# Optimization experiments

Measured on AMD Instinct MI355X. Metric: run time of the kernel, lower is better.

The kernel has to match this reference:

```python
import jax, jax.numpy as jnp
import numpy as np

B, S, C = 2, 2048, 1024
U, H = 1024, 16
FFH = int(U * 4.0)
NEG = -1e9
EPS = 1e-5


def setup_inputs() -> dict:
    key = jax.random.key(0)
    ks = jax.random.split(key, 16)
    w = lambda k, sh: jax.random.normal(k, sh, dtype=jnp.float32) * 0.02
    return {
        'x': jax.random.normal(ks[0], (B, S, C), dtype=jnp.float32),
        'wq': w(ks[1], (C, U)), 'bq': jnp.zeros((U,), jnp.float32),
        'wk': w(ks[2], (C, U)), 'bk': jnp.zeros((U,), jnp.float32),
        'wv': w(ks[3], (C, U)), 'bv': jnp.zeros((U,), jnp.float32),
        'wf1': w(ks[4], (U, FFH)), 'bf1': jnp.zeros((FFH,), jnp.float32),
        'wf2': w(ks[5], (FFH, U)), 'bf2': jnp.zeros((U,), jnp.float32),
        'ln_g': jnp.ones((S, U), jnp.float32), 'ln_b': jnp.zeros((S, U), jnp.float32),
        'ffln_g': jnp.ones((S, U), jnp.float32), 'ffln_b': jnp.zeros((S, U), jnp.float32),
    }


def _ln2d(x, g, b):
    # LayerNorm over last two dims ([len_ts, units]) as in nn.LayerNorm([S, U])
    m = jnp.mean(x, axis=(-2, -1), keepdims=True)
    v = jnp.mean(jnp.square(x - m), axis=(-2, -1), keepdims=True)
    return (x - m) * jax.lax.rsqrt(v + EPS) * g + b


def reference(x, wq, bq, wk, bk, wv, bv, wf1, bf1, wf2, bf2, ln_g, ln_b, ffln_g, ffln_b):
    dh = U // H
    Q = (x @ wq + bq).reshape(B, S, H, dh)
    K = (x @ wk + bk).reshape(B, S, H, dh)
    V = (x @ wv + bv).reshape(B, S, H, dh)
    scores = jnp.einsum('bqhd,bkhd->bhqk', Q, K) / jnp.sqrt(jnp.float32(dh))
    mask = jnp.tril(jnp.ones((S, S), dtype=bool))  # causal tril buffer
    scores = jnp.where(mask, scores, NEG)
    attn = jax.nn.softmax(scores, axis=-1)
    out = jnp.einsum('bhqk,bkhd->bqhd', attn, V).reshape(B, S, U)
    out = out + x  # residual
    out = _ln2d(out, ln_g, ln_b)
    ff = jax.nn.relu(out @ wf1 + bf1) @ wf2 + bf2
    out = _ln2d(out + ff, ffln_g, ffln_b)
    return out
```

## Files before the change

kernel.cpp:

```cpp
#include <hip/hip_runtime.h>
#include <hip/hip_bf16.h>

typedef short s16x8 __attribute__((ext_vector_type(8)));
typedef float f32x4 __attribute__((ext_vector_type(4)));
typedef float f32x16 __attribute__((ext_vector_type(16)));
typedef unsigned short u16x4 __attribute__((ext_vector_type(4)));
typedef unsigned u32x4 __attribute__((ext_vector_type(4)));

#define DEV static __device__ __forceinline__

DEV unsigned short f2bf(float f) {
  __hip_bfloat16 h = __float2bfloat16(f);
  return *reinterpret_cast<unsigned short*>(&h);
}
DEV float bf2f(unsigned short u) {
  union { unsigned u; float f; } v; v.u = (unsigned)u << 16; return v.f;
}

#define GLDS16(src, dst) \
  __builtin_amdgcn_global_load_lds((const __attribute__((address_space(1))) void*)(src), \
                                   (__attribute__((address_space(3))) void*)(dst), 16, 0, 0)

#define MFMA(a, b, c) __builtin_amdgcn_mfma_f32_16x16x32_bf16((a), (b), (c), 0, 0, 0)
#define MFMA32(a, b, c) __builtin_amdgcn_mfma_f32_32x32x16_bf16((a), (b), (c), 0, 0, 0)

__global__ __launch_bounds__(256) void k_f32_to_bf16(const float* __restrict__ in,
                                                     unsigned short* __restrict__ out, int n4) {
  int i = blockIdx.x * 256 + threadIdx.x;
  if (i >= n4) return;
  float4 v = ((const float4*)in)[i];
  u16x4 o; o.x = f2bf(v.x); o.y = f2bf(v.y); o.z = f2bf(v.z); o.w = f2bf(v.w);
  ((u16x4*)out)[i] = o;
}

__global__ __launch_bounds__(256) void k_transpose_w(const float* __restrict__ W,
                                                     unsigned short* __restrict__ Wt,
                                                     int K, int N, float scale) {
  __shared__ float t[64][65];
  int k0 = blockIdx.x * 64, n0 = blockIdx.y * 64;
  int tid = threadIdx.x;
#pragma unroll
  for (int i = 0; i < 16; ++i) {
    int idx = tid + i * 256; int r = idx >> 6, c = idx & 63;
    t[r][c] = W[(size_t)(k0 + r) * N + (n0 + c)];
  }
  __syncthreads();
#pragma unroll
  for (int i = 0; i < 16; ++i) {
    int idx = tid + i * 256; int r = idx >> 6, c = idx & 63;
    Wt[(size_t)(n0 + r) * K + (k0 + c)] = f2bf(t[c][r] * scale);
  }
}

__global__ void k_concat3(const float* __restrict__ a, const float* __restrict__ b,
                          const float* __restrict__ c, float* __restrict__ out, int n, float sa) {
  int i = blockIdx.x * 256 + threadIdx.x;
  if (i >= 3 * n) return;
  int j = (i < n) ? i : (i < 2 * n ? i - n : i - 2 * n);
  out[i] = (i < n) ? a[j] * sa : (i < 2 * n ? b[j] : c[j]);
}

template <int MODE>
__global__ __launch_bounds__(512, 2) void k_gemm8(
    const unsigned short* __restrict__ A, int lda,
    const unsigned short* __restrict__ Bt, int ldb,
    const float* __restrict__ bias,
    unsigned short* __restrict__ Cb, float* __restrict__ Cf, int ldc,
    int K, int nnt, size_t zstride,
    unsigned short* __restrict__ Cq, unsigned short* __restrict__ Ck,
    unsigned short* __restrict__ Cv) {
  __shared__ __align__(16) unsigned short As[2 * 2 * 8192];
  __shared__ __align__(16) unsigned short Bs[2 * 2 * 8192];
  int nwg = gridDim.x;
  int bid = blockIdx.x;
  int cpx = nwg >> 3;
  int swz = (bid & 7) * cpx + (bid >> 3);
  int mt = swz / nnt, nt = swz % nnt;
  int m0 = mt * 256, n0 = nt * 256;
  int tid = threadIdx.x, w = tid >> 6, l = tid & 63;
  int wm = (w >> 2) * 128, wn = (w & 3) * 64;
  int kb = blockIdx.z * K;

  int sr = tid >> 2;
  int gsrc = (tid & 3) ^ ((sr >> 1) & 3);
  const unsigned short* Ag0 = A + (size_t)(m0 + sr) * lda + kb + gsrc * 8;
  const unsigned short* Ag1 = Ag0 + (size_t)128 * lda;
  const unsigned short* Bg0 = Bt + (size_t)(n0 + sr) * ldb + kb + gsrc * 8;
  const unsigned short* Bg1 = Bg0 + (size_t)128 * ldb;

#define STG_A(t, kh) do { int _c = (t) * 64 + (kh) * 32; int _d = ((((t) & 1) * 2 + (kh)) * 8192); \
    GLDS16(Ag0 + _c, &As[_d + tid * 8]); GLDS16(Ag1 + _c, &As[_d + 4096 + tid * 8]); } while (0)
#define STG_B(t, kh) do { int _c = (t) * 64 + (kh) * 32; int _d = ((((t) & 1) * 2 + (kh)) * 8192); \
    GLDS16(Bg0 + _c, &Bs[_d + tid * 8]); GLDS16(Bg1 + _c, &Bs[_d + 4096 + tid * 8]); } while (0)

  int lswz = (l >> 1) & 3;
  int acol = ((l >> 4) ^ lswz) * 8;
  const unsigned short* Afr = &As[(wm + (l & 15)) * 32 + acol];
  const unsigned short* Bfr = &Bs[(wn + (l & 15)) * 32 + acol];

  f32x4 acc[8][4] = {};
  int nkt = K >> 6;

  STG_A(0, 0); STG_B(0, 0); STG_A(0, 1); STG_B(0, 1); STG_A(1, 0); STG_B(1, 0);
  asm volatile("s_waitcnt vmcnt(4)" ::: "memory");
  __builtin_amdgcn_s_barrier();
  __builtin_amdgcn_sched_barrier(0);

  for (int t = 0; t < nkt; ++t) {
    int cur = t & 1, rem = nkt - t;
    const unsigned short* ab = Afr + cur * 16384;
    const unsigned short* bb = Bfr + cur * 16384;
    s16x8 af[4], bf[4];
    if (t + 1 < nkt) STG_A(t + 1, 1);
#pragma unroll
    for (int nr = 0; nr < 4; ++nr) bf[nr] = *(const s16x8*)(bb + nr * 512);
#pragma unroll
    for (int mr = 0; mr < 4; ++mr) af[mr] = *(const s16x8*)(ab + mr * 512);
    __builtin_amdgcn_s_setprio(1);
#pragma unroll
    for (int mr = 0; mr < 4; ++mr)
#pragma unroll
      for (int nr = 0; nr < 4; ++nr)
        acc[mr][nr] = MFMA(af[mr], bf[nr], acc[mr][nr]);
    __builtin_amdgcn_s_setprio(0);
    if (t + 1 < nkt) STG_B(t + 1, 1);
#pragma unroll
    for (int mr = 0; mr < 4; ++mr) af[mr] = *(const s16x8*)(ab + 2048 + mr * 512);
    __builtin_amdgcn_s_setprio(1);
#pragma unroll
    for (int mr = 0; mr < 4; ++mr)
#pragma unroll
      for (int nr = 0; nr < 4; ++nr)
        acc[mr + 4][nr] = MFMA(af[mr], bf[nr], acc[mr + 4][nr]);
    __builtin_amdgcn_s_setprio(0);
    if (rem >= 2) { asm volatile("s_waitcnt vmcnt(4)" ::: "memory"); }
    else          { asm volatile("s_waitcnt vmcnt(0)" ::: "memory"); }
    __builtin_amdgcn_s_barrier();
    __builtin_amdgcn_sched_barrier(0);
    if (t + 2 < nkt) STG_A(t + 2, 0);
#pragma unroll
    for (int nr = 0; nr < 4; ++nr) bf[nr] = *(const s16x8*)(bb + 8192 + nr * 512);
#pragma unroll
    for (int mr = 0; mr < 4; ++mr) af[mr] = *(const s16x8*)(ab + 8192 + mr * 512);
    __builtin_amdgcn_s_setprio(1);
#pragma unroll
    for (int mr = 0; mr < 4; ++mr)
#pragma unroll
      for (int nr = 0; nr < 4; ++nr)
        acc[mr][nr] = MFMA(af[mr], bf[nr], acc[mr][nr]);
    __builtin_amdgcn_s_setprio(0);
    if (t + 2 < nkt) STG_B(t + 2, 0);
#pragma unroll
    for (int mr = 0; mr < 4; ++mr) af[mr] = *(const s16x8*)(ab + 8192 + 2048 + mr * 512);
    __builtin_amdgcn_s_setprio(1);
#pragma unroll
    for (int mr = 0; mr < 4; ++mr)
#pragma unroll
      for (int nr = 0; nr < 4; ++nr)
        acc[mr + 4][nr] = MFMA(af[mr], bf[nr], acc[mr + 4][nr]);
    __builtin_amdgcn_s_setprio(0);
    if (rem >= 3) { asm volatile("s_waitcnt vmcnt(4)" ::: "memory"); }
    else          { asm volatile("s_waitcnt vmcnt(0)" ::: "memory"); }
    __builtin_amdgcn_s_barrier();
    __builtin_amdgcn_sched_barrier(0);
  }
#undef STG_A
#undef STG_B

  if (MODE == 4) {
    if (nt < 8) {
      unsigned short* dst = (nt < 4) ? Cq : Ck;
      int cb = (nt < 4) ? 0 : 1024;
#pragma unroll
      for (int mr = 0; mr < 8; ++mr) {
        int rb = m0 + wm + mr * 16 + (l >> 4) * 4;
#pragma unroll
        for (int nr = 0; nr < 4; ++nr) {
          int col = n0 + wn + nr * 16 + (l & 15);
          float bv = bias[col];
#pragma unroll
          for (int j = 0; j < 4; ++j)
            dst[(size_t)(rb + j) * 1024 + (col - cb)] = f2bf(acc[mr][nr][j] + bv);
        }
      }
    } else {
#pragma unroll
      for (int mr = 0; mr < 8; ++mr) {
        int rb = m0 + wm + mr * 16 + (l >> 4) * 4;
        int b2 = rb >> 11, s2 = rb & 2047;
        int s2p = (s2 & ~12) | ((s2 & 4) << 1) | ((s2 & 8) >> 1);
#pragma unroll
        for (int nr = 0; nr < 4; ++nr) {
          int col2 = n0 - 2048 + wn + nr * 16 + (l & 15);
          float bv = bias[col2 + 2048];
          u16x4 pk;
#pragma unroll
          for (int j = 0; j < 4; ++j) ((unsigned short*)&pk)[j] = f2bf(acc[mr][nr][j] + bv);
          *(u16x4*)(Cv + ((size_t)((b2 * 16 + (col2 >> 6)) * 64 + (col2 & 63))) * 2048 + s2p) = pk;
        }
      }
    }
    return;
  }
  unsigned short* Cbz = (MODE == 3) ? (Cb + zstride * blockIdx.z) : Cb;
#pragma unroll
  for (int mr = 0; mr < 8; ++mr) {
    int rb = m0 + wm + mr * 16 + (l >> 4) * 4;
#pragma unroll
    for (int nr = 0; nr < 4; ++nr) {
      int col = n0 + wn + nr * 16 + (l & 15);
      float bv = (MODE == 3) ? 0.f : bias[col];
#pragma unroll
      for (int j = 0; j < 4; ++j) {
        float v = acc[mr][nr][j] + bv;
        size_t off = (size_t)(rb + j) * ldc + col;
        if (MODE == 1) v = fmaxf(v, 0.f);
        Cbz[off] = f2bf(v);
      }
    }
  }
}

__global__ __launch_bounds__(256) void k_ff2_reduce(
    unsigned short* __restrict__ slices, const float* __restrict__ bias,
    const unsigned short* __restrict__ resid, float* __restrict__ partials) {
  __shared__ float red[8];
  int i = blockIdx.x;
  size_t rb = (size_t)i * 4096;
  int c = threadIdx.x * 4;
  u16x4 a0 = *(const u16x4*)(slices + rb + c);
  u16x4 a1 = *(const u16x4*)(slices + rb + 1024 + c);
  u16x4 a2 = *(const u16x4*)(slices + rb + 2048 + c);
  u16x4 a3 = *(const u16x4*)(slices + rb + 3072 + c);
  float4 bv = *(const float4*)(bias + c);
  u16x4 rv = *(const u16x4*)(resid + (size_t)i * 1024 + c);
  float4 o;
  o.x = bf2f(a0.x) + bf2f(a1.x) + bf2f(a2.x) + bf2f(a3.x) + bv.x + bf2f(rv.x);
  o.y = bf2f(a0.y) + bf2f(a1.y) + bf2f(a2.y) + bf2f(a3.y) + bv.y + bf2f(rv.y);
  o.z = bf2f(a0.z) + bf2f(a1.z) + bf2f(a2.z) + bf2f(a3.z) + bv.z + bf2f(rv.z);
  o.w = bf2f(a0.w) + bf2f(a1.w) + bf2f(a2.w) + bf2f(a3.w) + bv.w + bf2f(rv.w);
  __syncthreads();
  *(float4*)((float*)slices + (size_t)i * 2048 + c) = o;
  float bsum = o.x + o.y + o.z + o.w;
  float bsq = o.x * o.x + o.y * o.y + o.z * o.z + o.w * o.w;
  int wv = threadIdx.x >> 6, lv = threadIdx.x & 63;
#pragma unroll
  for (int mk = 1; mk < 64; mk <<= 1) { bsum += __shfl_xor(bsum, mk); bsq += __shfl_xor(bsq, mk); }
  if (lv == 0) { red[wv] = bsum; red[4 + wv] = bsq; }
  __syncthreads();
  if (threadIdx.x == 0) {
    partials[i * 2] = red[0] + red[1] + red[2] + red[3];
    partials[i * 2 + 1] = red[4] + red[5] + red[6] + red[7];
  }
}

__global__ __launch_bounds__(128, 2) void k_attn(
    const unsigned short* __restrict__ Qg, const unsigned short* __restrict__ Kg,
    const unsigned short* __restrict__ Vt,
    const float* __restrict__ x, unsigned short* __restrict__ hpre,
    float* __restrict__ partials, int S, int H) {
  __shared__ __align__(16) unsigned short Ks[2][4096];
  __shared__ __align__(16) unsigned short Vs[2][4096];
  __shared__ float ascr[2][32];
  __shared__ float red[4];
  int bh = blockIdx.x, b = bh >> 4, h = bh & 15;
  const int nqt = S / 64;
  int qt = nqt - 1 - (int)blockIdx.y;
  int tid = threadIdx.x, w = tid >> 6, l = tid & 63;
  int lo = l & 31, hi5 = l >> 5;
  const int U = H * 64;
  const unsigned short* Qb = Qg + (size_t)(b * S) * 1024 + h * 64;
  const unsigned short* Kb = Kg + (size_t)(b * S) * 1024 + h * 64;
  const unsigned short* Vb = Vt + (size_t)bh * 64 * S;

  int sg_r[4], sg_c[4];
#pragma unroll
  for (int it = 0; it < 4; ++it) {
    int g = it * 128 + tid;
    sg_r[it] = g >> 3;
    sg_c[it] = ((g & 7) ^ ((g >> 3) & 7)) * 8;
  }
#define STG_K(kt) do { int _kn = (kt) * 64, _bf = (kt) & 1; \
    _Pragma("unroll") for (int it = 0; it < 4; ++it) \
      GLDS16(Kb + (size_t)(_kn + sg_r[it]) * 1024 + sg_c[it], &Ks[_bf][(it * 128 + tid) * 8]); } while (0)
#define STG_V(kt) do { int _kn = (kt) * 64, _bf = (kt) & 1; \
    _Pragma("unroll") for (int it = 0; it < 4; ++it) \
      GLDS16(Vb + (size_t)sg_r[it] * S + _kn + sg_c[it], &Vs[_bf][(it * 128 + tid) * 8]); } while (0)

  int qrow = qt * 64 + w * 32 + lo;
  s16x8 qf[4];
#pragma unroll
  for (int s = 0; s < 4; ++s)
    qf[s] = *(const s16x8*)(Qb + (size_t)qrow * 1024 + s * 16 + hi5 * 8);

  int krow[16];
#pragma unroll
  for (int r = 0; r < 16; ++r) krow[r] = (r & 3) + 8 * (r >> 2) + 4 * hi5;

  f32x16 o0 = {}, o1 = {};
  float m = -1e30f, lsum = 0.f;
  f32x16 scA0, scA1, scB0, scB1;

#define QK_T(S0, S1, T) do { \
    S0 = (f32x16)(0.0f); S1 = (f32x16)(0.0f); \
    const unsigned short* _kp = &Ks[(T) & 1][0]; \
    __builtin_amdgcn_s_setprio(1); \
    _Pragma("unroll") for (int s = 0; s < 4; ++s) { \
      int gc = ((2 * s + hi5) ^ (lo & 7)) * 8; \
      s16x8 kf0 = *(const s16x8*)&_kp[lo * 64 + gc]; \
      s16x8 kf1 = *(const s16x8*)&_kp[(32 + lo) * 64 + gc]; \
      S0 = MFMA32(kf0, qf[s], S0); \
      S1 = MFMA32(kf1, qf[s], S1); } \
    __builtin_amdgcn_s_setprio(0); } while (0)

#define SMPV(S0, S1, T, DOMASK) do { \
    if (DOMASK) { int wq = w * 32 + lo; \
      _Pragma("unroll") for (int r = 0; r < 16; ++r) { \
        if (krow[r] > wq) S0[r] = -1e30f; \
        if (krow[r] + 32 > wq) S1[r] = -1e30f; } } \
    float mx = S0[0]; \
    _Pragma("unroll") for (int r = 1; r < 16; ++r) mx = fmaxf(mx, S0[r]); \
    _Pragma("unroll") for (int r = 0; r < 16; ++r) mx = fmaxf(mx, S1[r]); \
    mx = fmaxf(mx, __shfl_xor(mx, 32)); \
    if (__ballot(mx > m + 11.5415603f)) { \
      float mnew = fmaxf(m, mx); \
      float alpha = __builtin_amdgcn_exp2f(m - mnew); \
      m = mnew; lsum *= alpha; \
      if (l < 32) ascr[w][lo] = alpha; \
      _Pragma("unroll") for (int r = 0; r < 16; ++r) { \
        float aj = ascr[w][krow[r]]; o0[r] *= aj; o1[r] *= aj; } } \
    float rs = 0.f; unsigned wk0[8], wk1[8]; \
    _Pragma("unroll") for (int j = 0; j < 8; ++j) { \
      float p0 = __builtin_amdgcn_exp2f(S0[2 * j] - m); \
      float p1 = __builtin_amdgcn_exp2f(S0[2 * j + 1] - m); \
      rs += p0 + p1; wk0[j] = (unsigned)f2bf(p0) | ((unsigned)f2bf(p1) << 16); \
      float p2 = __builtin_amdgcn_exp2f(S1[2 * j] - m); \
      float p3 = __builtin_amdgcn_exp2f(S1[2 * j + 1] - m); \
      rs += p2 + p3; wk1[j] = (unsigned)f2bf(p2) | ((unsigned)f2bf(p3) << 16); } \
    rs += __shfl_xor(rs, 32); lsum += rs; \
    __builtin_amdgcn_s_setprio(1); \
    _Pragma("unroll") for (int s = 0; s < 4; ++s) { \
      u32x4 paw; \
      if (s == 0)      { paw.x = wk0[0]; paw.y = wk0[1]; paw.z = wk0[2]; paw.w = wk0[3]; } \
      else if (s == 1) { paw.x = wk0[4]; paw.y = wk0[5]; paw.z = wk0[6]; paw.w = wk0[7]; } \
      else if (s == 2) { paw.x = wk1[0]; paw.y = wk1[1]; paw.z = wk1[2]; paw.w = wk1[3]; } \
      else             { paw.x = wk1[4]; paw.y = wk1[5]; paw.z = wk1[6]; paw.w = wk1[7]; } \
      s16x8 pa = *(s16x8*)&paw; \
      int gc = ((2 * s + hi5) ^ (lo & 7)) * 8; \
      s16x8 vf0 = *(const s16x8*)&Vs[(T) & 1][lo * 64 + gc]; \
      s16x8 vf1 = *(const s16x8*)&Vs[(T) & 1][(32 + lo) * 64 + gc]; \
      o0 = MFMA32(pa, vf0, o0); \
      o1 = MFMA32(pa, vf1, o1); } \
    __builtin_amdgcn_s_setprio(0); \
  } while (0)

#define BODY(O0, O1, I0, I1, T) do { \
    asm volatile("s_waitcnt vmcnt(4)" ::: "memory"); \
    __builtin_amdgcn_s_barrier(); \
    __builtin_amdgcn_sched_barrier(0); \
    if ((T) + 1 <= qt) STG_K((T) + 1); \
    QK_T(O0, O1, (T)); \
    SMPV(I0, I1, (T) - 1, false); \
    asm volatile("s_waitcnt lgkmcnt(0)" ::: "memory"); \
    __builtin_amdgcn_sched_barrier(0); \
    __builtin_amdgcn_s_barrier(); \
    __builtin_amdgcn_sched_barrier(0); \
    if ((T) + 1 <= qt) STG_V((T) + 1); \
  } while (0)

  STG_K(0); STG_V(0);
  if (qt >= 1) {
    STG_K(1); STG_V(1);
    asm volatile("s_waitcnt vmcnt(8)" ::: "memory");
  } else {
    asm volatile("s_waitcnt vmcnt(4)" ::: "memory");
  }
  __builtin_amdgcn_s_barrier();
  __builtin_amdgcn_sched_barrier(0);
  QK_T(scA0, scA1, 0);
  asm volatile("s_waitcnt lgkmcnt(0)" ::: "memory");
  __builtin_amdgcn_sched_barrier(0);

  int t = 1;
  for (; t + 1 <= qt; t += 2) {
    BODY(scB0, scB1, scA0, scA1, t);
    BODY(scA0, scA1, scB0, scB1, t + 1);
  }
  if (t <= qt) {
    BODY(scB0, scB1, scA0, scA1, t);
    asm volatile("s_waitcnt vmcnt(0)" ::: "memory");
    __builtin_amdgcn_sched_barrier(0);
    SMPV(scB0, scB1, qt, true);
  } else {
    asm volatile("s_waitcnt vmcnt(0)" ::: "memory");
    __builtin_amdgcn_sched_barrier(0);
    SMPV(scA0, scA1, qt, true);
  }

  if (l < 32) ascr[w][lo] = 1.f / lsum;
  float bsum = 0.f, bsq = 0.f;
  unsigned short* hb = hpre + (size_t)(b * S) * U + h * 64;
  const float* xb = x + (size_t)(b * S) * U + h * 64;
#pragma unroll
  for (int r = 0; r < 16; ++r) {
    float inv = ascr[w][krow[r]];
    int srow = qt * 64 + w * 32 + krow[r];
    size_t base = (size_t)srow * U + lo;
    float v0 = o0[r] * inv + xb[base];
    float v1 = o1[r] * inv + xb[base + 32];
    hb[base] = f2bf(v0);
    hb[base + 32] = f2bf(v1);
    bsum += v0 + v1; bsq += v0 * v0 + v1 * v1;
  }
#pragma unroll
  for (int mk = 1; mk < 64; mk <<= 1) { bsum += __shfl_xor(bsum, mk); bsq += __shfl_xor(bsq, mk); }
  if (l == 0) { red[w * 2] = bsum; red[w * 2 + 1] = bsq; }
  __syncthreads();
  if (tid == 0) {
    int pi = b * (H * nqt) + h * nqt + qt;
    partials[pi * 2] = red[0] + red[2];
    partials[pi * 2 + 1] = red[1] + red[3];
  }
#undef STG_K
#undef STG_V
#undef QK_T
#undef SMPV
#undef BODY
}

__global__ __launch_bounds__(256) void k_ln_stats(const float* __restrict__ partials, int nper,
                                                  float* __restrict__ stats, float invN) {
  int b = blockIdx.x, tid = threadIdx.x;
  float s = 0.f, q = 0.f;
  for (int i = tid; i < nper; i += 256) { s += partials[(b * nper + i) * 2]; q += partials[(b * nper + i) * 2 + 1]; }
#pragma unroll
  for (int mk = 1; mk < 64; mk <<= 1) { s += __shfl_xor(s, mk); q += __shfl_xor(q, mk); }
  __shared__ float red[8];
  int w = tid >> 6, l = tid & 63;
  if (l == 0) { red[w] = s; red[4 + w] = q; }
  __syncthreads();
  if (tid == 0) {
    s = red[0] + red[1] + red[2] + red[3];
    q = red[4] + red[5] + red[6] + red[7];
    float m = s * invN, var = q * invN - m * m;
    stats[b * 2] = m; stats[b * 2 + 1] = rsqrtf(var + 1e-5f);
  }
}

__global__ __launch_bounds__(256) void k_ln_apply_b(
    const unsigned short* __restrict__ src, const float* __restrict__ stats,
    const float* __restrict__ g, const float* __restrict__ bt,
    unsigned short* __restrict__ outb, int SU) {
  int b = blockIdx.y;
  int idx = (blockIdx.x * 256 + threadIdx.x) * 4;
  float m = stats[b * 2], r = stats[b * 2 + 1];
  u16x4 v4 = *(const u16x4*)(src + (size_t)b * SU + idx);
  float4 gg = *(const float4*)(g + idx);
  float4 bb = *(const float4*)(bt + idx);
  u16x4 ob;
  ob.x = f2bf((bf2f(v4.x) - m) * r * gg.x + bb.x);
  ob.y = f2bf((bf2f(v4.y) - m) * r * gg.y + bb.y);
  ob.z = f2bf((bf2f(v4.z) - m) * r * gg.z + bb.z);
  ob.w = f2bf((bf2f(v4.w) - m) * r * gg.w + bb.w);
  *(u16x4*)(outb + (size_t)b * SU + idx) = ob;
}

__global__ __launch_bounds__(256) void k_ln_apply2(
    const float* __restrict__ src, const float* __restrict__ stats,
    const float* __restrict__ g, const float* __restrict__ bt,
    float* __restrict__ outf) {
  int b = blockIdx.y;
  int row = blockIdx.x;
  int grow = b * 2048 + row;
  int c = threadIdx.x * 4;
  float m = stats[b * 2], r = stats[b * 2 + 1];
  float4 v = *(const float4*)(src + (size_t)grow * 2048 + c);
  float4 gg = *(const float4*)(g + (size_t)row * 1024 + c);
  float4 bb = *(const float4*)(bt + (size_t)row * 1024 + c);
  float4 o;
  o.x = (v.x - m) * r * gg.x + bb.x;
  o.y = (v.y - m) * r * gg.y + bb.y;
  o.z = (v.z - m) * r * gg.z + bb.z;
  o.w = (v.w - m) * r * gg.w + bb.w;
  *(float4*)(outf + (size_t)grow * 1024 + c) = o;
}

extern "C" void kernel_launch(void* const* d_in, const int* in_sizes, int n_in,
                              void* d_out, int out_size, void* d_ws, size_t ws_size,
                              hipStream_t stream) {
  (void)in_sizes; (void)n_in; (void)out_size; (void)ws_size;
  const int S = 2048, H = 16;
  const float* x   = (const float*)d_in[0];
  const float* wq  = (const float*)d_in[1];
  const float* bq  = (const float*)d_in[2];
  const float* wk  = (const float*)d_in[3];
  const float* bk  = (const float*)d_in[4];
  const float* wv  = (const float*)d_in[5];
  const float* bv  = (const float*)d_in[6];
  const float* wf1 = (const float*)d_in[7];
  const float* bf1 = (const float*)d_in[8];
  const float* wf2 = (const float*)d_in[9];
  const float* bf2 = (const float*)d_in[10];
  const float* lng = (const float*)d_in[11];
  const float* lnb = (const float*)d_in[12];
  const float* ffg = (const float*)d_in[13];
  const float* ffb = (const float*)d_in[14];

  char* ws = (char*)d_ws;
  unsigned short* wqkvT = (unsigned short*)(ws);
  unsigned short* wf1T  = (unsigned short*)(ws + 6291456);
  unsigned short* wf2T  = (unsigned short*)(ws + 14680064);
  unsigned short* xb    = (unsigned short*)(ws + 23068672);
  unsigned short* qb    = (unsigned short*)(ws + 31457280);
  unsigned short* kbuf  = (unsigned short*)(ws + 39845888);
  unsigned short* vt    = (unsigned short*)(ws + 56623104);
  unsigned short* h1b   = (unsigned short*)(ws + 65011712);
  unsigned short* hpreb = (unsigned short*)(ws + 73400320);
  unsigned short* ff2s  = (unsigned short*)(ws + 73400320);
  unsigned short* f1b   = (unsigned short*)(ws + 23068672);
  float* biasqkv        = (float*)(ws + 106954752);
  float* part_attn      = (float*)(ws + 106967040);
  float* stats1         = (float*)(ws + 106977280);
  float* ffpart2        = (float*)(ws);
  float* stats2         = (float*)(ws + 65536);

  const float qscale = 0.125f * 1.44269504f;
  k_f32_to_bf16<<<4096, 256, 0, stream>>>(x, xb, 4096 * 1024 / 4);
  k_transpose_w<<<dim3(16, 16), 256, 0, stream>>>(wq, wqkvT, 1024, 1024, qscale);
  k_transpose_w<<<dim3(16, 16), 256, 0, stream>>>(wk, wqkvT + 1024 * 1024, 1024, 1024, 1.0f);
  k_transpose_w<<<dim3(16, 16), 256, 0, stream>>>(wv, wqkvT + 2048 * 1024, 1024, 1024, 1.0f);
  k_transpose_w<<<dim3(16, 64), 256, 0, stream>>>(wf1, wf1T, 1024, 4096, 1.0f);
  k_transpose_w<<<dim3(64, 16), 256, 0, stream>>>(wf2, wf2T, 4096, 1024, 1.0f);
  k_concat3<<<12, 256, 0, stream>>>(bq, bk, bv, biasqkv, 1024, qscale);

  k_gemm8<4><<<dim3(192, 1, 1), 512, 0, stream>>>(xb, 1024, wqkvT, 1024, biasqkv,
      nullptr, nullptr, 0, 1024, 12, 0, qb, kbuf, vt);

  k_attn<<<dim3(32, 32), 128, 0, stream>>>(qb, kbuf, vt, x, hpreb, part_attn, S, H);

  k_ln_stats<<<2, 256, 0, stream>>>(part_attn, 512, stats1, 1.f / (2048.f * 1024.f));
  k_ln_apply_b<<<dim3(2048, 2), 256, 0, stream>>>(hpreb, stats1, lng, lnb, h1b, S * 1024);

  k_gemm8<1><<<dim3(256, 1, 1), 512, 0, stream>>>(h1b, 1024, wf1T, 1024, bf1,
      f1b, nullptr, 4096, 1024, 16, 0, nullptr, nullptr, nullptr);

  k_gemm8<3><<<dim3(64, 1, 4), 512, 0, stream>>>(f1b, 4096, wf2T, 4096, nullptr,
      ff2s, nullptr, 4096, 1024, 4, 1024, nullptr, nullptr, nullptr);

  k_ff2_reduce<<<4096, 256, 0, stream>>>(ff2s, bf2, h1b, ffpart2);

  k_ln_stats<<<2, 256, 0, stream>>>(ffpart2, 2048, stats2, 1.f / (2048.f * 1024.f));
  k_ln_apply2<<<dim3(2048, 2), 256, 0, stream>>>((float*)ff2s, stats2, ffg, ffb, (float*)d_out);
}
```

Baseline: 233.4 us.

## Pair causal attention q-tiles per block and merge QKV weight transposes

The attention kernel now launches half as many blocks. Each block handles two query tiles, a long one (nqt-1-y) and a short one (y), which evens out the per-block work under the causal mask. Separately, the three Q/K/V weight transposes are fused into one launch using a z-dimension grid, saving two kernel launches. The trade-off is fewer blocks in flight (512 instead of 1024) and a second serial pass per block, which could lower occupancy and latency hiding.

```diff
diff --git a/kernel.cpp b/kernel.cpp
--- a/kernel.cpp
+++ b/kernel.cpp
@@ -49,6 +49,29 @@
   for (int i = 0; i < 16; ++i) {
     int idx = tid + i * 256; int r = idx >> 6, c = idx & 63;
     Wt[(size_t)(n0 + r) * K + (k0 + c)] = f2bf(t[c][r] * scale);
+  }
+}
+
+__global__ __launch_bounds__(256) void k_transpose_w3(
+    const float* __restrict__ W0, const float* __restrict__ W1,
+    const float* __restrict__ W2, unsigned short* __restrict__ Wt, float s0) {
+  __shared__ float t[64][65];
+  int z = blockIdx.z;
+  const float* W = (z == 0) ? W0 : (z == 1) ? W1 : W2;
+  float scale = (z == 0) ? s0 : 1.0f;
+  unsigned short* dst = Wt + (size_t)z * 1024 * 1024;
+  int k0 = blockIdx.x * 64, n0 = blockIdx.y * 64;
+  int tid = threadIdx.x;
+#pragma unroll
+  for (int i = 0; i < 16; ++i) {
+    int idx = tid + i * 256; int r = idx >> 6, c = idx & 63;
+    t[r][c] = W[(size_t)(k0 + r) * 1024 + (n0 + c)];
+  }
+  __syncthreads();
+#pragma unroll
+  for (int i = 0; i < 16; ++i) {
+    int idx = tid + i * 256; int r = idx >> 6, c = idx & 63;
+    dst[(size_t)(n0 + r) * 1024 + (k0 + c)] = f2bf(t[c][r] * scale);
   }
 }
 
@@ -265,7 +288,6 @@
   __shared__ float red[4];
   int bh = blockIdx.x, b = bh >> 4, h = bh & 15;
   const int nqt = S / 64;
-  int qt = nqt - 1 - (int)blockIdx.y;
   int tid = threadIdx.x, w = tid >> 6, l = tid & 63;
   int lo = l & 31, hi5 = l >> 5;
   const int U = H * 64;
@@ -287,19 +309,9 @@
     _Pragma("unroll") for (int it = 0; it < 4; ++it) \
       GLDS16(Vb + (size_t)sg_r[it] * S + _kn + sg_c[it], &Vs[_bf][(it * 128 + tid) * 8]); } while (0)
 
-  int qrow = qt * 64 + w * 32 + lo;
-  s16x8 qf[4];
-#pragma unroll
-  for (int s = 0; s < 4; ++s)
-    qf[s] = *(const s16x8*)(Qb + (size_t)qrow * 1024 + s * 16 + hi5 * 8);
-
   int krow[16];
 #pragma unroll
   for (int r = 0; r < 16; ++r) krow[r] = (r & 3) + 8 * (r >> 2) + 4 * hi5;
-
-  f32x16 o0 = {}, o1 = {};
-  float m = -1e30f, lsum = 0.f;
-  f32x16 scA0, scA1, scB0, scB1;
 
 #define QK_T(S0, S1, T) do { \
     S0 = (f32x16)(0.0f); S1 = (f32x16)(0.0f); \
@@ -368,58 +380,73 @@
     if ((T) + 1 <= qt) STG_V((T) + 1); \
   } while (0)
 
-  STG_K(0); STG_V(0);
-  if (qt >= 1) {
-    STG_K(1); STG_V(1);
-    asm volatile("s_waitcnt vmcnt(8)" ::: "memory");
-  } else {
-    asm volatile("s_waitcnt vmcnt(4)" ::: "memory");
-  }
-  __builtin_amdgcn_s_barrier();
-  __builtin_amdgcn_sched_barrier(0);
-  QK_T(scA0, scA1, 0);
-  asm volatile("s_waitcnt lgkmcnt(0)" ::: "memory");
-  __builtin_amdgcn_sched_barrier(0);
-
-  int t = 1;
-  for (; t + 1 <= qt; t += 2) {
-    BODY(scB0, scB1, scA0, scA1, t);
-    BODY(scA0, scA1, scB0, scB1, t + 1);
-  }
-  if (t <= qt) {
-    BODY(scB0, scB1, scA0, scA1, t);
-    asm volatile("s_waitcnt vmcnt(0)" ::: "memory");
+  for (int pass = 0; pass < 2; ++pass) {
+    int qt = (pass == 0) ? (nqt - 1 - (int)blockIdx.y) : (int)blockIdx.y;
+
+    int qrow = qt * 64 + w * 32 + lo;
+    s16x8 qf[4];
+#pragma unroll
+    for (int s = 0; s < 4; ++s)
+      qf[s] = *(const s16x8*)(Qb + (size_t)qrow * 1024 + s * 16 + hi5 * 8);
+
+    f32x16 o0 = {}, o1 = {};
+    float m = -1e30f, lsum = 0.f;
+    f32x16 scA0, scA1, scB0, scB1;
+
+    STG_K(0); STG_V(0);
+    if (qt >= 1) {
+      STG_K(1); STG_V(1);
+      asm volatile("s_waitcnt vmcnt(8)" ::: "memory");
+    } else {
+      asm volatile("s_waitcnt vmcnt(4)" ::: "memory");
+    }
+    __builtin_amdgcn_s_barrier();
     __builtin_amdgcn_sched_barrier(0);
-    SMPV(scB0, scB1, qt, true);
-  } else {
-    asm volatile("s_waitcnt vmcnt(0)" ::: "memory");
+    QK_T(scA0, scA1, 0);
+    asm volatile("s_waitcnt lgkmcnt(0)" ::: "memory");
     __builtin_amdgcn_sched_barrier(0);
-    SMPV(scA0, scA1, qt, true);
-  }
-
-  if (l < 32) ascr[w][lo] = 1.f / lsum;
-  float bsum = 0.f, bsq = 0.f;
-  unsigned short* hb = hpre + (size_t)(b * S) * U + h * 64;
-  const float* xb = x + (size_t)(b * S) * U + h * 64;
-#pragma unroll
-  for (int r = 0; r < 16; ++r) {
-    float inv = ascr[w][krow[r]];
-    int srow = qt * 64 + w * 32 + krow[r];
-    size_t base = (size_t)srow * U + lo;
-    float v0 = o0[r] * inv + xb[base];
-    float v1 = o1[r] * inv + xb[base + 32];
-    hb[base] = f2bf(v0);
-    hb[base + 32] = f2bf(v1);
-    bsum += v0 + v1; bsq += v0 * v0 + v1 * v1;
-  }
-#pragma unroll
-  for (int mk = 1; mk < 64; mk <<= 1) { bsum += __shfl_xor(bsum, mk); bsq += __shfl_xor(bsq, mk); }
-  if (l == 0) { red[w * 2] = bsum; red[w * 2 + 1] = bsq; }
-  __syncthreads();
-  if (tid == 0) {
-    int pi = b * (H * nqt) + h * nqt + qt;
-    partials[pi * 2] = red[0] + red[2];
-    partials[pi * 2 + 1] = red[1] + red[3];
+
+    int t = 1;
+    for (; t + 1 <= qt; t += 2) {
+      BODY(scB0, scB1, scA0, scA1, t);
+      BODY(scA0, scA1, scB0, scB1, t + 1);
+    }
+    if (t <= qt) {
+      BODY(scB0, scB1, scA0, scA1, t);
+      asm volatile("s_waitcnt vmcnt(0)" ::: "memory");
+      __builtin_amdgcn_sched_barrier(0);
+      SMPV(scB0, scB1, qt, true);
+    } else {
+      asm volatile("s_waitcnt vmcnt(0)" ::: "memory");
+      __builtin_amdgcn_sched_barrier(0);
+      SMPV(scA0, scA1, qt, true);
+    }
+
+    if (l < 32) ascr[w][lo] = 1.f / lsum;
+    float bsum = 0.f, bsq = 0.f;
+    unsigned short* hb = hpre + (size_t)(b * S) * U + h * 64;
+    const float* xb = x + (size_t)(b * S) * U + h * 64;
+#pragma unroll
+    for (int r = 0; r < 16; ++r) {
+      float inv = ascr[w][krow[r]];
+      int srow = qt * 64 + w * 32 + krow[r];
+      size_t base = (size_t)srow * U + lo;
+      float v0 = o0[r] * inv + xb[base];
+      float v1 = o1[r] * inv + xb[base + 32];
+      hb[base] = f2bf(v0);
+      hb[base + 32] = f2bf(v1);
+      bsum += v0 + v1; bsq += v0 * v0 + v1 * v1;
+    }
+#pragma unroll
+    for (int mk = 1; mk < 64; mk <<= 1) { bsum += __shfl_xor(bsum, mk); bsq += __shfl_xor(bsq, mk); }
+    if (l == 0) { red[w * 2] = bsum; red[w * 2 + 1] = bsq; }
+    __syncthreads();
+    if (tid == 0) {
+      int pi = b * (H * nqt) + h * nqt + qt;
+      partials[pi * 2] = red[0] + red[2];
+      partials[pi * 2 + 1] = red[1] + red[3];
+    }
+    __syncthreads();
   }
 #undef STG_K
 #undef STG_V
@@ -526,9 +553,7 @@
 
   const float qscale = 0.125f * 1.44269504f;
   k_f32_to_bf16<<<4096, 256, 0, stream>>>(x, xb, 4096 * 1024 / 4);
-  k_transpose_w<<<dim3(16, 16), 256, 0, stream>>>(wq, wqkvT, 1024, 1024, qscale);
-  k_transpose_w<<<dim3(16, 16), 256, 0, stream>>>(wk, wqkvT + 1024 * 1024, 1024, 1024, 1.0f);
-  k_transpose_w<<<dim3(16, 16), 256, 0, stream>>>(wv, wqkvT + 2048 * 1024, 1024, 1024, 1.0f);
+  k_transpose_w3<<<dim3(16, 16, 3), 256, 0, stream>>>(wq, wk, wv, wqkvT, qscale);
   k_transpose_w<<<dim3(16, 64), 256, 0, stream>>>(wf1, wf1T, 1024, 4096, 1.0f);
   k_transpose_w<<<dim3(64, 16), 256, 0, stream>>>(wf2, wf2T, 4096, 1024, 1.0f);
   k_concat3<<<12, 256, 0, stream>>>(bq, bk, bv, biasqkv, 1024, qscale);
@@ -536,7 +561,7 @@
   k_gemm8<4><<<dim3(192, 1, 1), 512, 0, stream>>>(xb, 1024, wqkvT, 1024, biasqkv,
       nullptr, nullptr, 0, 1024, 12, 0, qb, kbuf, vt);
 
-  k_attn<<<dim3(32, 32), 128, 0, stream>>>(qb, kbuf, vt, x, hpreb, part_attn, S, H);
+  k_attn<<<dim3(32, 16), 128, 0, stream>>>(qb, kbuf, vt, x, hpreb, part_attn, S, H);
 
   k_ln_stats<<<2, 256, 0, stream>>>(part_attn, 512, stats1, 1.f / (2048.f * 1024.f));
   k_ln_apply_b<<<dim3(2048, 2), 256, 0, stream>>>(hpreb, stats1, lng, lnb, h1b, S * 1024);
```

New measurement: 244.3 us. 4.7% more time.
